# Kernel tuning notes

Measured on AMD Instinct MI355X. Metric: run time of the kernel, lower is better.

The kernel has to match this reference:

```python
import jax, jax.numpy as jnp
import numpy as np


def setup_inputs() -> dict:
    key = jax.random.key(0)
    k1, k2, k3, k4 = jax.random.split(key, 4)
    T, H, I, E, K = 4096, 1024, 1024, 8, 2
    hidden_states = jax.random.normal(k1, (T, H), dtype=jnp.float32)
    router_logits = jax.random.normal(k2, (T, E), dtype=jnp.float32)
    # fused gate+up projection: [E, H, 2*I]; down projection: [E, I, H]
    up_weight = jax.random.normal(k3, (E, H, 2 * I), dtype=jnp.float32) * 0.02
    down_weight = jax.random.normal(k4, (E, I, H), dtype=jnp.float32) * 0.02
    return {"hidden_states": hidden_states, "router_logits": router_logits,
            "up_weight": up_weight, "down_weight": down_weight, "topk": K}


def reference(hidden_states, router_logits, up_weight, down_weight, topk):
    T, H = hidden_states.shape
    E = up_weight.shape[0]
    I = down_weight.shape[1]
    K = topk
    # select_experts: softmax over all experts, top-k, renormalize weights
    probs = jax.nn.softmax(router_logits, axis=-1)
    topk_w, topk_ids = jax.lax.top_k(probs, K)               # [T, K]
    topk_w = topk_w / jnp.sum(topk_w, axis=-1, keepdims=True)
    # expand tokens: each token is dispatched K times (grouped-GEMM operand)
    xk = jnp.repeat(hidden_states, K, axis=0)                # [T*K, H]
    flat_ids = topk_ids.reshape(-1)                          # [T*K]
    acc = jnp.zeros((T * K, H), dtype=hidden_states.dtype)
    for e in range(E):  # fixed small expert loop (grouped GEMM semantics)
        mask = (flat_ids == e).astype(hidden_states.dtype)[:, None]
        xe = xk * mask                                       # zero out non-e tokens
        gu = xe @ up_weight[e]                               # [T*K, 2I]
        h = jax.nn.silu(gu[:, :I]) * gu[:, I:]               # gated SiLU
        acc = acc + h @ down_weight[e]                       # [T*K, H]
    # combine: weighted sum over the K expert slots (reduce step)
    out = jnp.einsum('tk,tkh->th', topk_w, acc.reshape(T, K, H))
    return out
```

## Files before the change

kernel.cpp:

```cpp
#include <hip/hip_runtime.h>
#include <hip/hip_bf16.h>


#define T_TOK 4096
#define HDIM  1024
#define NEXP  8
#define RROWS (T_TOK * 2)
#define MAXPE T_TOK

typedef unsigned short u16;
typedef short v8s __attribute__((ext_vector_type(8)));
typedef float v4f __attribute__((ext_vector_type(4)));
typedef __attribute__((address_space(3))) unsigned int as3_u32;
typedef const __attribute__((address_space(1))) unsigned int as1_u32c;

__device__ __forceinline__ float b2f(u16 u) {
    union { unsigned int i; float f; } v; v.i = ((unsigned int)u) << 16; return v.f;
}
__device__ __forceinline__ u16 f2b(float f) {
    union { float f; unsigned int i; } v; v.f = f;
    unsigned int x = v.i;
    return (u16)((x + 0x7FFFu + ((x >> 16) & 1u)) >> 16);
}
__device__ __forceinline__ unsigned int pack2(float a, float b) {
    return (unsigned int)f2b(a) | ((unsigned int)f2b(b) << 16);
}
__device__ __forceinline__ void stage16(const u16* g, u16* l) {
    __builtin_amdgcn_global_load_lds((as1_u32c*)g, (as3_u32*)l, 16, 0, 0);
}

__global__ void router_kernel(const float* __restrict__ logits,
                              int* __restrict__ ids, float* __restrict__ wts) {
    int t = blockIdx.x * blockDim.x + threadIdx.x;
    if (t >= T_TOK) return;
    float4 a = *(const float4*)(logits + t * NEXP);
    float4 b = *(const float4*)(logits + t * NEXP + 4);
    float l[NEXP] = {a.x, a.y, a.z, a.w, b.x, b.y, b.z, b.w};
    int i0 = 0;
#pragma unroll
    for (int i = 1; i < NEXP; i++) if (l[i] > l[i0]) i0 = i;
    int i1 = (i0 == 0) ? 1 : 0;
#pragma unroll
    for (int i = 0; i < NEXP; i++) if (i != i0 && l[i] > l[i1]) i1 = i;
    float w0 = 1.0f / (1.0f + expf(l[i1] - l[i0]));
    ids[2 * t] = i0;     ids[2 * t + 1] = i1;
    wts[2 * t] = w0;     wts[2 * t + 1] = 1.0f - w0;
}

__global__ void bucket_kernel(const int* __restrict__ ids,
                              int* __restrict__ counts, int* __restrict__ rowbuf) {
    int r = blockIdx.x * blockDim.x + threadIdx.x;
    if (r >= RROWS) return;
    int e = ids[r];
    int pos = atomicAdd(&counts[e], 1);
    rowbuf[e * MAXPE + pos] = r;
}

__global__ void cvtX_kernel(const float* __restrict__ X, u16* __restrict__ Xb) {
    int i = (blockIdx.x * 256 + threadIdx.x) * 4;
    float4 f = *(const float4*)(X + i);
    uint2 o; o.x = pack2(f.x, f.y); o.y = pack2(f.z, f.w);
    *(uint2*)(Xb + i) = o;
}

__global__ void cvtW_kernel(const float* __restrict__ W, u16* __restrict__ Wt, int N) {
    __shared__ __align__(16) u16 tile[64 * 72];
    int e = blockIdx.z;
    int n0 = blockIdx.x * 64, k0 = blockIdx.y * 64;
    const float* Wb = W + (size_t)e * 1024 * N;
    u16* Wtb = Wt + (size_t)e * N * 1024;
    int r = threadIdx.x >> 4, c4 = (threadIdx.x & 15) * 4;
#pragma unroll
    for (int j = 0; j < 4; j++) {
        int k = r + j * 16;
        float4 f = *(const float4*)(Wb + (size_t)(k0 + k) * N + n0 + c4);
        tile[(c4 + 0) * 72 + k] = f2b(f.x);
        tile[(c4 + 1) * 72 + k] = f2b(f.y);
        tile[(c4 + 2) * 72 + k] = f2b(f.z);
        tile[(c4 + 3) * 72 + k] = f2b(f.w);
    }
    __syncthreads();
    int n = threadIdx.x >> 2, kc = (threadIdx.x & 3) * 16;
    uint4 v0 = *(const uint4*)&tile[n * 72 + kc];
    uint4 v1 = *(const uint4*)&tile[n * 72 + kc + 8];
    u16* dst = Wtb + (size_t)(n0 + n) * 1024 + k0 + kc;
    *(uint4*)dst = v0;
    *(uint4*)(dst + 8) = v1;
}

template<int PHASE>
__global__ __launch_bounds__(256)
void mfma_gemm(const u16* __restrict__ A, const u16* __restrict__ Bt,
               u16* __restrict__ H, float* __restrict__ OUT,
               const int* __restrict__ counts, const int* __restrict__ rowbuf,
               const float* __restrict__ wts) {
    const int e = blockIdx.z, rt = blockIdx.y, ct = blockIdx.x;
    const int cnt = counts[e];
    if (rt * 128 >= cnt) return;
    const int tid = threadIdx.x;
    const int lane = tid & 63, wave = tid >> 6;

    __shared__ __align__(16) u16 sA[128 * 64];
    __shared__ __align__(16) u16 sB[128 * 64];
    __shared__ int srid[128];

    if (tid < 128) {
        int idx = rt * 128 + tid;
        srid[tid] = (idx < cnt) ? rowbuf[e * MAXPE + idx] : -1;
    }
    __syncthreads();

    const int lrow = lane >> 3;
    const int lchunk = (lane & 7) ^ lrow;
    const u16* aPtr[4]; const u16* bPtr[4];
    u16 *aDst[4], *bDst[4];
#pragma unroll
    for (int p = 0; p < 4; p++) {
        int region = p * 4 + wave;
        int r = region * 8 + lrow;
        int rid = srid[r];
        int arow = (rid < 0) ? 0 : (PHASE == 1 ? (rid >> 1) : rid);
        aPtr[p] = A + (size_t)arow * 1024 + lchunk * 8;
        aDst[p] = sA + region * 512 + lane * 8;
        int n;
        if (PHASE == 1) n = (r < 64) ? (ct * 64 + r) : (1024 + ct * 64 + (r - 64));
        else            n = ct * 128 + r;
        bPtr[p] = Bt + (size_t)e * (PHASE == 1 ? 2048 : 1024) * 1024
                     + (size_t)n * 1024 + lchunk * 8;
        bDst[p] = sB + region * 512 + lane * 8;
    }

    const int quad = lane >> 4, mr = lane & 15;
    const int swA = mr & 7;
    const v4f zf = {0.f, 0.f, 0.f, 0.f};
    v4f acc[2][8];
#pragma unroll
    for (int i = 0; i < 2; i++)
#pragma unroll
        for (int j = 0; j < 8; j++) acc[i][j] = zf;

    for (int kk = 0; kk < 16; kk++) {
        __syncthreads();
#pragma unroll
        for (int p = 0; p < 4; p++) {
            stage16(aPtr[p] + kk * 64, aDst[p]);
            stage16(bPtr[p] + kk * 64, bDst[p]);
        }
        __syncthreads();
#pragma unroll
        for (int kh = 0; kh < 2; kh++) {
            const int c = kh * 4 + quad;
            v8s a0 = *(const v8s*)(sA + (wave * 32 + mr) * 64 + ((c ^ swA) * 8));
            v8s a1 = *(const v8s*)(sA + (wave * 32 + 16 + mr) * 64 + ((c ^ swA) * 8));
#pragma unroll
            for (int nf = 0; nf < 8; nf++) {
                v8s b = *(const v8s*)(sB + (nf * 16 + mr) * 64 + ((c ^ swA) * 8));
                acc[0][nf] = __builtin_amdgcn_mfma_f32_16x16x32_bf16(a0, b, acc[0][nf], 0, 0, 0);
                acc[1][nf] = __builtin_amdgcn_mfma_f32_16x16x32_bf16(a1, b, acc[1][nf], 0, 0, 0);
            }
        }
    }

#pragma unroll
    for (int mf = 0; mf < 2; mf++) {
#pragma unroll
        for (int reg = 0; reg < 4; reg++) {
            int rl = wave * 32 + mf * 16 + quad * 4 + reg;
            int grow = srid[rl];
            if (grow < 0) continue;
            if (PHASE == 1) {
                size_t base = (size_t)grow * 1024 + ct * 64 + mr;
#pragma unroll
                for (int nf = 0; nf < 4; nf++) {
                    float g = acc[mf][nf][reg], u = acc[mf][nf + 4][reg];
                    H[base + nf * 16] = f2b((g / (1.0f + expf(-g))) * u);
                }
            } else {
                float w = wts[grow];
                size_t base = (size_t)(grow >> 1) * 1024 + ct * 128 + mr;
#pragma unroll
                for (int nf = 0; nf < 8; nf++)
                    atomicAdd(&OUT[base + nf * 16], w * acc[mf][nf][reg]);
            }
        }
    }
}

template<int GATED, int AF32>
__global__ __launch_bounds__(256)
void moe_gemm_kernel(const void* __restrict__ Av,
                     const float* __restrict__ B,
                     u16* __restrict__ C,
                     const int* __restrict__ counts,
                     const int* __restrict__ rowbuf,
                     int rowShift, int NB) {
    const int e   = blockIdx.z;
    const int cnt = counts[e];
    const int rt  = blockIdx.y;
    if (rt * 128 >= cnt) return;
    const int ct  = blockIdx.x;
    const int tid = threadIdx.x;

    __shared__ __align__(16) u16 sA[128 * 40];
    __shared__ __align__(16) u16 sB[(GATED ? 2 : 1) * 64 * 40];
    __shared__ int srid[128];

    if (tid < 128) {
        int idx = rt * 128 + tid;
        srid[tid] = (idx < cnt) ? rowbuf[e * MAXPE + idx] : -1;
    }
    __syncthreads();

    const int ar = tid >> 1, ac = (tid & 1) * 16;
    int arid = srid[ar];
    const float* aSrcF = 0; const u16* aSrcH = 0;
    if (arid >= 0) {
        if (AF32) aSrcF = (const float*)Av + (size_t)(arid >> rowShift) * HDIM + ac;
        else      aSrcH = (const u16*)Av + (size_t)(arid >> rowShift) * HDIM + ac;
    }
    u16* aDst = sA + ar * 40 + ac;

    const int kq2 = (tid >> 4) * 2, n4 = (tid & 15) * 4;
    const float* bSrcG = B + (size_t)e * 1024 * NB + (size_t)kq2 * NB + ct * 64 + n4;
    const float* bSrcU = bSrcG + 1024;

    const int lane = tid & 63, wave = tid >> 6;
    const int quad = lane >> 4, mr = lane & 15;

    const v4f zf = {0.f, 0.f, 0.f, 0.f};
    v4f accG[2][4], accU[2][4];
#pragma unroll
    for (int i = 0; i < 2; i++)
#pragma unroll
        for (int j = 0; j < 4; j++) { accG[i][j] = zf; accU[i][j] = zf; }

    for (int kk = 0; kk < HDIM / 32; kk++) {
        uint4 aw0 = make_uint4(0, 0, 0, 0), aw1 = make_uint4(0, 0, 0, 0);
        if (AF32) {
            if (aSrcF) {
                float4 f0 = *(const float4*)(aSrcF + kk * 32);
                float4 f1 = *(const float4*)(aSrcF + kk * 32 + 4);
                float4 f2 = *(const float4*)(aSrcF + kk * 32 + 8);
                float4 f3 = *(const float4*)(aSrcF + kk * 32 + 12);
                aw0 = make_uint4(pack2(f0.x, f0.y), pack2(f0.z, f0.w),
                                 pack2(f1.x, f1.y), pack2(f1.z, f1.w));
                aw1 = make_uint4(pack2(f2.x, f2.y), pack2(f2.z, f2.w),
                                 pack2(f3.x, f3.y), pack2(f3.z, f3.w));
            }
        } else {
            if (aSrcH) {
                aw0 = *(const uint4*)(aSrcH + kk * 32);
                aw1 = *(const uint4*)(aSrcH + kk * 32 + 8);
            }
        }
        const size_t bOff = (size_t)kk * 32 * NB;
        float4 g0 = *(const float4*)(bSrcG + bOff);
        float4 g1 = *(const float4*)(bSrcG + bOff + NB);
        float4 u0 = make_float4(0, 0, 0, 0), u1 = make_float4(0, 0, 0, 0);
        if (GATED) {
            u0 = *(const float4*)(bSrcU + bOff);
            u1 = *(const float4*)(bSrcU + bOff + NB);
        }

        __syncthreads();
        *(uint4*)aDst = aw0;
        *(uint4*)(aDst + 8) = aw1;
        {
            const float gx[4] = {g0.x, g0.y, g0.z, g0.w};
            const float gy[4] = {g1.x, g1.y, g1.z, g1.w};
#pragma unroll
            for (int j = 0; j < 4; j++)
                *(unsigned int*)&sB[(n4 + j) * 40 + kq2] = pack2(gx[j], gy[j]);
            if (GATED) {
                const float ux[4] = {u0.x, u0.y, u0.z, u0.w};
                const float uy[4] = {u1.x, u1.y, u1.z, u1.w};
#pragma unroll
                for (int j = 0; j < 4; j++)
                    *(unsigned int*)&sB[64 * 40 + (n4 + j) * 40 + kq2] = pack2(ux[j], uy[j]);
            }
        }
        __syncthreads();

        v8s af0 = *(const v8s*)(sA + (wave * 32 + mr) * 40 + quad * 8);
        v8s af1 = *(const v8s*)(sA + (wave * 32 + 16 + mr) * 40 + quad * 8);
#pragma unroll
        for (int nf = 0; nf < 4; nf++) {
            v8s bg = *(const v8s*)(sB + (nf * 16 + mr) * 40 + quad * 8);
            accG[0][nf] = __builtin_amdgcn_mfma_f32_16x16x32_bf16(af0, bg, accG[0][nf], 0, 0, 0);
            accG[1][nf] = __builtin_amdgcn_mfma_f32_16x16x32_bf16(af1, bg, accG[1][nf], 0, 0, 0);
            if (GATED) {
                v8s bu = *(const v8s*)(sB + 64 * 40 + (nf * 16 + mr) * 40 + quad * 8);
                accU[0][nf] = __builtin_amdgcn_mfma_f32_16x16x32_bf16(af0, bu, accU[0][nf], 0, 0, 0);
                accU[1][nf] = __builtin_amdgcn_mfma_f32_16x16x32_bf16(af1, bu, accU[1][nf], 0, 0, 0);
            }
        }
    }

#pragma unroll
    for (int mf = 0; mf < 2; mf++) {
#pragma unroll
        for (int reg = 0; reg < 4; reg++) {
            int rl = wave * 32 + mf * 16 + quad * 4 + reg;
            int grow = srid[rl];
            if (grow < 0) continue;
            size_t base = (size_t)grow * 1024 + ct * 64 + mr;
#pragma unroll
            for (int nf = 0; nf < 4; nf++) {
                float g = accG[mf][nf][reg];
                float val;
                if (GATED) {
                    float u = accU[mf][nf][reg];
                    val = (g / (1.0f + expf(-g))) * u;
                } else {
                    val = g;
                }
                C[base + nf * 16] = f2b(val);
            }
        }
    }
}

__global__ void combine_kernel(const u16* __restrict__ accb,
                               const float* __restrict__ wts,
                               float* __restrict__ out) {
    int g = blockIdx.x * blockDim.x + threadIdx.x;
    int t = g >> 8;
    int c = (g & 255) * 4;
    float w0 = wts[2 * t], w1 = wts[2 * t + 1];
    ushort4 a = *(const ushort4*)(accb + (size_t)(2 * t) * 1024 + c);
    ushort4 b = *(const ushort4*)(accb + (size_t)(2 * t + 1) * 1024 + c);
    float4 o;
    o.x = w0 * b2f(a.x) + w1 * b2f(b.x);
    o.y = w0 * b2f(a.y) + w1 * b2f(b.y);
    o.z = w0 * b2f(a.z) + w1 * b2f(b.z);
    o.w = w0 * b2f(a.w) + w1 * b2f(b.w);
    *(float4*)(out + (size_t)t * 1024 + c) = o;
}

extern "C" void kernel_launch(void* const* d_in, const int* in_sizes, int n_in,
                              void* d_out, int out_size, void* d_ws, size_t ws_size,
                              hipStream_t stream) {
    const float *X = 0, *RL = 0, *WU = 0, *WD = 0;
    for (int i = 0; i < n_in; i++) {
        switch (in_sizes[i]) {
            case T_TOK * HDIM:        X  = (const float*)d_in[i]; break;
            case T_TOK * NEXP:        RL = (const float*)d_in[i]; break;
            case NEXP * HDIM * 2048:  WU = (const float*)d_in[i]; break;
            case NEXP * HDIM * 1024:  WD = (const float*)d_in[i]; break;
            default: break;
        }
    }
    if (!X)  X  = (const float*)d_in[0];
    if (!RL) RL = (const float*)d_in[1];
    if (!WU) WU = (const float*)d_in[2];
    if (!WD) WD = (const float*)d_in[3];
    float* OUT = (float*)d_out;

    char* ws = (char*)d_ws;
    int*   ids    = (int*)(ws + 0);
    float* wts    = (float*)(ws + 32768);
    int*   counts = (int*)(ws + 65536);
    int*   rowbuf = (int*)(ws + 65792);
    u16* Xb   = (u16*)(ws + 196864);
    u16* WtU  = (u16*)(ws + 8585472);
    u16* WtD  = (u16*)(ws + 42139904);
    u16* HbufF= (u16*)(ws + 58917120);
    const size_t needFast = 75694336ull;
    u16* Hbuf = (u16*)(ws + 196864);
    u16* Acc  = (u16*)(ws + 196864 + 16777216);
    const size_t needA = 196864 + 2 * 16777216ull;

    hipMemsetAsync(counts, 0, NEXP * sizeof(int), stream);
    router_kernel<<<T_TOK / 256, 256, 0, stream>>>(RL, ids, wts);
    bucket_kernel<<<RROWS / 256, 256, 0, stream>>>(ids, counts, rowbuf);

    if (ws_size >= needFast) {
        hipMemsetAsync(d_out, 0, (size_t)out_size * sizeof(float), stream);
        cvtX_kernel<<<T_TOK * HDIM / 1024, 256, 0, stream>>>(X, Xb);
        cvtW_kernel<<<dim3(32, 16, NEXP), 256, 0, stream>>>(WU, WtU, 2048);
        cvtW_kernel<<<dim3(16, 16, NEXP), 256, 0, stream>>>(WD, WtD, 1024);
        mfma_gemm<1><<<dim3(16, 32, NEXP), 256, 0, stream>>>(
            Xb, WtU, HbufF, OUT, counts, rowbuf, wts);
        mfma_gemm<2><<<dim3(8, 32, NEXP), 256, 0, stream>>>(
            HbufF, WtD, HbufF, OUT, counts, rowbuf, wts);
    } else {
        moe_gemm_kernel<1, 1><<<dim3(16, 32, NEXP), 256, 0, stream>>>(
            (const void*)X, WU, Hbuf, counts, rowbuf, 1, 2048);
        moe_gemm_kernel<0, 0><<<dim3(16, 32, NEXP), 256, 0, stream>>>(
            (const void*)Hbuf, WD, Acc, counts, rowbuf, 0, 1024);
        combine_kernel<<<T_TOK, 256, 0, stream>>>(Acc, wts, OUT);
    }
}
```

Baseline: 296.3 us.

## Fuse prep kernels and remap GEMM blocks across XCDs for L2 reuse

Merges the router, bucket, X conversion and output zeroing into one prep kernel, and the two weight-conversion launches into one, so fewer launches and memsets run. The GEMM grids become 1D, with block indices remapped so blocks sharing an expert and column tile land on the same XCD (round-robin by index & 7), aiming for better L2 reuse of weights. Bucketing order of rows within an expert changes, and the atomics in the prep kernel are now interleaved with conversion work.

```diff
diff --git a/kernel.cpp b/kernel.cpp
--- a/kernel.cpp
+++ b/kernel.cpp
@@ -29,46 +29,49 @@
     __builtin_amdgcn_global_load_lds((as1_u32c*)g, (as3_u32*)l, 16, 0, 0);
 }
 
-__global__ void router_kernel(const float* __restrict__ logits,
-                              int* __restrict__ ids, float* __restrict__ wts) {
-    int t = blockIdx.x * blockDim.x + threadIdx.x;
-    if (t >= T_TOK) return;
-    float4 a = *(const float4*)(logits + t * NEXP);
-    float4 b = *(const float4*)(logits + t * NEXP + 4);
-    float l[NEXP] = {a.x, a.y, a.z, a.w, b.x, b.y, b.z, b.w};
-    int i0 = 0;
-#pragma unroll
-    for (int i = 1; i < NEXP; i++) if (l[i] > l[i0]) i0 = i;
-    int i1 = (i0 == 0) ? 1 : 0;
-#pragma unroll
-    for (int i = 0; i < NEXP; i++) if (i != i0 && l[i] > l[i1]) i1 = i;
-    float w0 = 1.0f / (1.0f + expf(l[i1] - l[i0]));
-    ids[2 * t] = i0;     ids[2 * t + 1] = i1;
-    wts[2 * t] = w0;     wts[2 * t + 1] = 1.0f - w0;
-}
-
-__global__ void bucket_kernel(const int* __restrict__ ids,
-                              int* __restrict__ counts, int* __restrict__ rowbuf) {
-    int r = blockIdx.x * blockDim.x + threadIdx.x;
-    if (r >= RROWS) return;
-    int e = ids[r];
-    int pos = atomicAdd(&counts[e], 1);
-    rowbuf[e * MAXPE + pos] = r;
-}
-
-__global__ void cvtX_kernel(const float* __restrict__ X, u16* __restrict__ Xb) {
-    int i = (blockIdx.x * 256 + threadIdx.x) * 4;
+__global__ __launch_bounds__(256)
+void prep_kernel(const float* __restrict__ X, const float* __restrict__ RL,
+                 u16* __restrict__ Xb, float* __restrict__ outZ,
+                 int* __restrict__ ids, float* __restrict__ wts,
+                 int* __restrict__ counts, int* __restrict__ rowbuf) {
+    int gid = blockIdx.x * 256 + threadIdx.x;
+    int i = gid * 4;
     float4 f = *(const float4*)(X + i);
     uint2 o; o.x = pack2(f.x, f.y); o.y = pack2(f.z, f.w);
     *(uint2*)(Xb + i) = o;
-}
-
-__global__ void cvtW_kernel(const float* __restrict__ W, u16* __restrict__ Wt, int N) {
+    float4 z = {0.f, 0.f, 0.f, 0.f};
+    *(float4*)(outZ + i) = z;
+
+    if (gid < T_TOK) {
+        int t = gid;
+        float4 a = *(const float4*)(RL + t * NEXP);
+        float4 b = *(const float4*)(RL + t * NEXP + 4);
+        float l[NEXP] = {a.x, a.y, a.z, a.w, b.x, b.y, b.z, b.w};
+        int i0 = 0;
+#pragma unroll
+        for (int q = 1; q < NEXP; q++) if (l[q] > l[i0]) i0 = q;
+        int i1 = (i0 == 0) ? 1 : 0;
+#pragma unroll
+        for (int q = 0; q < NEXP; q++) if (q != i0 && l[q] > l[i1]) i1 = q;
+        float w0 = 1.0f / (1.0f + expf(l[i1] - l[i0]));
+        ids[2 * t] = i0;     ids[2 * t + 1] = i1;
+        wts[2 * t] = w0;     wts[2 * t + 1] = 1.0f - w0;
+        int p0 = atomicAdd(&counts[i0], 1);
+        rowbuf[i0 * MAXPE + p0] = 2 * t;
+        int p1 = atomicAdd(&counts[i1], 1);
+        rowbuf[i1 * MAXPE + p1] = 2 * t + 1;
+    }
+}
+
+__global__ void cvtW_all(const float* __restrict__ WU, const float* __restrict__ WD,
+                         u16* __restrict__ WtU, u16* __restrict__ WtD) {
     __shared__ __align__(16) u16 tile[64 * 72];
     int e = blockIdx.z;
-    int n0 = blockIdx.x * 64, k0 = blockIdx.y * 64;
-    const float* Wb = W + (size_t)e * 1024 * N;
-    u16* Wtb = Wt + (size_t)e * N * 1024;
+    const float* Wb; u16* Wtb; int N;
+    int bx = blockIdx.x;
+    if (bx < 32) { Wb = WU + (size_t)e * 1024 * 2048; Wtb = WtU + (size_t)e * 2048 * 1024; N = 2048; }
+    else         { Wb = WD + (size_t)e * 1024 * 1024; Wtb = WtD + (size_t)e * 1024 * 1024; N = 1024; bx -= 32; }
+    int n0 = bx * 64, k0 = blockIdx.y * 64;
     int r = threadIdx.x >> 4, c4 = (threadIdx.x & 15) * 4;
 #pragma unroll
     for (int j = 0; j < 4; j++) {
@@ -94,7 +97,11 @@
                u16* __restrict__ H, float* __restrict__ OUT,
                const int* __restrict__ counts, const int* __restrict__ rowbuf,
                const float* __restrict__ wts) {
-    const int e = blockIdx.z, rt = blockIdx.y, ct = blockIdx.x;
+    const int bi = blockIdx.x;
+    const int xcd = bi & 7, kb = bi >> 3;
+    int e, ct, rt;
+    if (PHASE == 1) { int p = (kb & 15) * 8 + xcd; e = p >> 4; ct = p & 15; rt = kb >> 4; }
+    else            { int p = (kb & 7) * 8 + xcd;  e = p >> 3; ct = p & 7;  rt = kb >> 3; }
     const int cnt = counts[e];
     if (rt * 128 >= cnt) return;
     const int tid = threadIdx.x;
@@ -184,6 +191,33 @@
             }
         }
     }
+}
+
+__global__ void router_kernel(const float* __restrict__ logits,
+                              int* __restrict__ ids, float* __restrict__ wts) {
+    int t = blockIdx.x * blockDim.x + threadIdx.x;
+    if (t >= T_TOK) return;
+    float4 a = *(const float4*)(logits + t * NEXP);
+    float4 b = *(const float4*)(logits + t * NEXP + 4);
+    float l[NEXP] = {a.x, a.y, a.z, a.w, b.x, b.y, b.z, b.w};
+    int i0 = 0;
+#pragma unroll
+    for (int i = 1; i < NEXP; i++) if (l[i] > l[i0]) i0 = i;
+    int i1 = (i0 == 0) ? 1 : 0;
+#pragma unroll
+    for (int i = 0; i < NEXP; i++) if (i != i0 && l[i] > l[i1]) i1 = i;
+    float w0 = 1.0f / (1.0f + expf(l[i1] - l[i0]));
+    ids[2 * t] = i0;     ids[2 * t + 1] = i1;
+    wts[2 * t] = w0;     wts[2 * t + 1] = 1.0f - w0;
+}
+
+__global__ void bucket_kernel(const int* __restrict__ ids,
+                              int* __restrict__ counts, int* __restrict__ rowbuf) {
+    int r = blockIdx.x * blockDim.x + threadIdx.x;
+    if (r >= RROWS) return;
+    int e = ids[r];
+    int pos = atomicAdd(&counts[e], 1);
+    rowbuf[e * MAXPE + pos] = r;
 }
 
 template<int GATED, int AF32>
@@ -368,22 +402,18 @@
     const size_t needFast = 75694336ull;
     u16* Hbuf = (u16*)(ws + 196864);
     u16* Acc  = (u16*)(ws + 196864 + 16777216);
-    const size_t needA = 196864 + 2 * 16777216ull;
 
     hipMemsetAsync(counts, 0, NEXP * sizeof(int), stream);
-    router_kernel<<<T_TOK / 256, 256, 0, stream>>>(RL, ids, wts);
-    bucket_kernel<<<RROWS / 256, 256, 0, stream>>>(ids, counts, rowbuf);
 
     if (ws_size >= needFast) {
-        hipMemsetAsync(d_out, 0, (size_t)out_size * sizeof(float), stream);
-        cvtX_kernel<<<T_TOK * HDIM / 1024, 256, 0, stream>>>(X, Xb);
-        cvtW_kernel<<<dim3(32, 16, NEXP), 256, 0, stream>>>(WU, WtU, 2048);
-        cvtW_kernel<<<dim3(16, 16, NEXP), 256, 0, stream>>>(WD, WtD, 1024);
-        mfma_gemm<1><<<dim3(16, 32, NEXP), 256, 0, stream>>>(
-            Xb, WtU, HbufF, OUT, counts, rowbuf, wts);
-        mfma_gemm<2><<<dim3(8, 32, NEXP), 256, 0, stream>>>(
-            HbufF, WtD, HbufF, OUT, counts, rowbuf, wts);
+        prep_kernel<<<T_TOK * HDIM / 1024, 256, 0, stream>>>(
+            X, RL, Xb, OUT, ids, wts, counts, rowbuf);
+        cvtW_all<<<dim3(48, 16, NEXP), 256, 0, stream>>>(WU, WD, WtU, WtD);
+        mfma_gemm<1><<<4096, 256, 0, stream>>>(Xb, WtU, HbufF, OUT, counts, rowbuf, wts);
+        mfma_gemm<2><<<2048, 256, 0, stream>>>(HbufF, WtD, HbufF, OUT, counts, rowbuf, wts);
     } else {
+        router_kernel<<<T_TOK / 256, 256, 0, stream>>>(RL, ids, wts);
+        bucket_kernel<<<RROWS / 256, 256, 0, stream>>>(ids, counts, rowbuf);
         moe_gemm_kernel<1, 1><<<dim3(16, 32, NEXP), 256, 0, stream>>>(
             (const void*)X, WU, Hbuf, counts, rowbuf, 1, 2048);
         moe_gemm_kernel<0, 0><<<dim3(16, 32, NEXP), 256, 0, stream>>>(
```

Result: faster. 285.6 us (-3.6%).
